# Kernel optimization log

Hardware: AMD Instinct MI355X
Metric: run time of the kernel (lower is better)

## Reference

```python
import jax, jax.numpy as jnp
import numpy as np

B, S, H, I, E = 4, 2048, 1024, 2048, 8
TOP_K = 2
INIT = 0.02


def setup_inputs() -> dict:
    key = jax.random.key(0)
    kx, kg, k1, k2, k3 = jax.random.split(key, 5)
    hidden_states = jax.random.normal(kx, (B, S, H), dtype=jnp.float32)
    gate_w = jax.random.normal(kg, (H, E), dtype=jnp.float32) * INIT
    w_gate = jax.random.normal(k1, (E, H, I), dtype=jnp.float32) * INIT  # per-expert gate_proj
    w_up = jax.random.normal(k2, (E, H, I), dtype=jnp.float32) * INIT    # per-expert up_proj
    w_down = jax.random.normal(k3, (E, I, H), dtype=jnp.float32) * INIT  # per-expert down_proj
    return {"hidden_states": hidden_states, "gate_w": gate_w,
            "w_gate": w_gate, "w_up": w_up, "w_down": w_down}


def reference(hidden_states, gate_w, w_gate, w_up, w_down):
    # Router: logits kept in float32 (original promotes to >= float32)
    router_logits = jnp.einsum('bsh,he->bse', hidden_states, gate_w).astype(jnp.float32)
    routing_weights, selected_experts = jax.lax.top_k(router_logits, k=TOP_K)
    routing_weights = jax.nn.softmax(routing_weights, axis=-1)  # [B,S,K]
    # Per-token combine weight for every expert (sum over the k slots that picked it)
    one_hot = jax.nn.one_hot(selected_experts, E, dtype=routing_weights.dtype)  # [B,S,K,E]
    combine = jnp.einsum('bske,bsk->bse', one_hot, routing_weights)  # [B,S,E]
    # Compute-all-experts dense MLP (faithful to the original per-expert loop, vectorized over E)
    gate = jax.nn.gelu(jnp.einsum('bsh,ehi->ebsi', hidden_states, w_gate), approximate=True)
    up = jnp.einsum('bsh,ehi->ebsi', hidden_states, w_up)
    expert_out = jnp.einsum('ebsi,eih->ebsh', gate * up, w_down)  # [E,B,S,H]
    final_hidden_state = jnp.einsum('bse,ebsh->bsh', combine, expert_out)
    return final_hidden_state, router_logits
```

## Files before the change

### kernel.cpp

```cpp
#include <hip/hip_runtime.h>
#include <hip/hip_bf16.h>

#define TOKENS  8192
#define HDIM    1024
#define IDIM    2048
#define NEXP    8
#define NPAIRS  16384

typedef __attribute__((ext_vector_type(8))) short bf16x8;
typedef __attribute__((ext_vector_type(4))) float f32x4;
typedef __attribute__((ext_vector_type(8))) unsigned short u16x8;

__device__ __forceinline__ unsigned short f2b(float f){
  unsigned u = __float_as_uint(f);
  u += 0x7fff + ((u >> 16) & 1);
  return (unsigned short)(u >> 16);
}

__device__ __forceinline__ void gload16(const void* g, void* l){
  __builtin_amdgcn_global_load_lds(
    (const __attribute__((address_space(1))) unsigned int*)g,
    (__attribute__((address_space(3))) unsigned int*)l, 16, 0, 0);
}

__device__ __forceinline__ float gelu_tanh(float x){
  float x3 = x*x*x;
  float t = tanhf(0.7978845608028654f*(x + 0.044715f*x3));
  return 0.5f*x*(1.0f+t);
}


__global__ void conv_hs_k(const float4* __restrict__ src, ushort4* __restrict__ dst, int n4){
  int i = blockIdx.x*blockDim.x + threadIdx.x;
  if (i >= n4) return;
  float4 v = src[i];
  ushort4 o;
  o.x = f2b(v.x); o.y = f2b(v.y); o.z = f2b(v.z); o.w = f2b(v.w);
  dst[i] = o;
}

__global__ __launch_bounds__(256)
void transpose_conv_k(const float* __restrict__ src, unsigned short* __restrict__ dst,
                      int R, int C){
  __shared__ float tile[64][65];
  size_t base = (size_t)blockIdx.z * R * C;
  const int t = threadIdx.x;
  const int x0 = blockIdx.x*64, y0 = blockIdx.y*64;
  const int rl = t >> 4, c4 = (t & 15) * 4;
  #pragma unroll
  for (int i=0;i<4;++i){
    int r = i*16 + rl;
    float4 v = *(const float4*)&src[base + (size_t)(y0 + r)*C + x0 + c4];
    tile[r][c4+0]=v.x; tile[r][c4+1]=v.y; tile[r][c4+2]=v.z; tile[r][c4+3]=v.w;
  }
  __syncthreads();
  const int c = t >> 2, r0 = (t & 3)*16;
  size_t ob = base + (size_t)(x0 + c)*R + y0;
  #pragma unroll
  for (int v=0; v<2; ++v){
    int r = r0 + v*8;
    u16x8 o;
    #pragma unroll
    for (int j=0;j<8;++j) o[j] = f2b(tile[r+j][c]);
    *(u16x8*)&dst[ob + r] = o;
  }
}


__global__ void router_k(const float* __restrict__ hs, const float* __restrict__ gw,
                         float* __restrict__ lo, int4* __restrict__ tokinfo){
  int wid  = (blockIdx.x*blockDim.x + threadIdx.x) >> 6;
  int lane = threadIdx.x & 63;
  const float* h = hs + (size_t)wid*HDIM;
  float a0=0,a1=0,a2=0,a3=0,a4=0,a5=0,a6=0,a7=0;
  for (int i = lane; i < HDIM; i += 64){
    float x = h[i];
    const float4 g0 = *(const float4*)(gw + (size_t)i*NEXP);
    const float4 g1 = *(const float4*)(gw + (size_t)i*NEXP + 4);
    a0 += x*g0.x; a1 += x*g0.y; a2 += x*g0.z; a3 += x*g0.w;
    a4 += x*g1.x; a5 += x*g1.y; a6 += x*g1.z; a7 += x*g1.w;
  }
  #pragma unroll
  for (int off = 32; off; off >>= 1){
    a0 += __shfl_xor(a0, off); a1 += __shfl_xor(a1, off);
    a2 += __shfl_xor(a2, off); a3 += __shfl_xor(a3, off);
    a4 += __shfl_xor(a4, off); a5 += __shfl_xor(a5, off);
    a6 += __shfl_xor(a6, off); a7 += __shfl_xor(a7, off);
  }
  if (lane == 0){
    float v[8] = {a0,a1,a2,a3,a4,a5,a6,a7};
    float* lp = lo + (size_t)wid*NEXP;
    #pragma unroll
    for (int e=0;e<8;++e) lp[e] = v[e];
    int e0 = 0; float b0 = v[0];
    #pragma unroll
    for (int e=1;e<8;++e){ if (v[e] > b0){ b0 = v[e]; e0 = e; } }
    int e1 = 0; float b1 = -1e30f;
    #pragma unroll
    for (int e=0;e<8;++e){ if (e != e0 && v[e] > b1){ b1 = v[e]; e1 = e; } }
    float ex = expf(b1 - b0);
    float w0 = 1.0f/(1.0f+ex);
    float w1 = ex/(1.0f+ex);
    tokinfo[wid] = make_int4(e0, e1, __float_as_int(w0), __float_as_int(w1));
  }
}

__global__ __launch_bounds__(256)
void hist_k(const int4* __restrict__ tokinfo, int* __restrict__ ctl){
  __shared__ int h[8];
  if (threadIdx.x < 8) h[threadIdx.x] = 0;
  __syncthreads();
  int4 ti = tokinfo[blockIdx.x*256 + threadIdx.x];
  atomicAdd(&h[ti.x], 1); atomicAdd(&h[ti.y], 1);
  __syncthreads();
  if (threadIdx.x < 8) atomicAdd(&ctl[threadIdx.x], h[threadIdx.x]);
}

__global__ void scan_k(int* ctl){
  if (threadIdx.x == 0){
    int s = 0;
    #pragma unroll
    for (int e=0;e<NEXP;++e){ ctl[16+e] = s; s += ctl[e]; }
  }
}

__global__ __launch_bounds__(256)
void assign_k(const int4* __restrict__ tokinfo, int* ctl,
              int* __restrict__ ptok, float* __restrict__ pw,
              int2* __restrict__ ppos){
  __shared__ int wcnt0[4][8], wcnt1[4][8];
  __shared__ int woff0[4][8], woff1[4][8];
  __shared__ int btot0[8], blkbase[8];
  const int tid = threadIdx.x, lane = tid & 63, wv = tid >> 6;
  const int tok = blockIdx.x*256 + tid;
  int4 ti = tokinfo[tok];
  const unsigned long long below = (1ull << lane) - 1ull;
  int r0 = 0, r1 = 0;
  #pragma unroll
  for (int e=0;e<8;++e){
    unsigned long long b0 = __ballot(ti.x == e);
    unsigned long long b1 = __ballot(ti.y == e);
    if (ti.x == e) r0 = __popcll(b0 & below);
    if (ti.y == e) r1 = __popcll(b1 & below);
    if (lane == 0){ wcnt0[wv][e] = __popcll(b0); wcnt1[wv][e] = __popcll(b1); }
  }
  __syncthreads();
  if (tid < 8){
    const int e = tid;
    int s0 = 0, s1 = 0;
    #pragma unroll
    for (int w=0;w<4;++w){ woff0[w][e] = s0; s0 += wcnt0[w][e]; }
    btot0[e] = s0;
    #pragma unroll
    for (int w=0;w<4;++w){ woff1[w][e] = s1; s1 += wcnt1[w][e]; }
    blkbase[e] = atomicAdd(&ctl[8+e], s0 + s1);
  }
  __syncthreads();
  const int e0 = ti.x, e1 = ti.y;
  int p0 = ctl[16+e0] + blkbase[e0] + woff0[wv][e0] + r0;
  int p1 = ctl[16+e1] + blkbase[e1] + btot0[e1] + woff1[wv][e1] + r1;
  ptok[p0] = tok; pw[p0] = __int_as_float(ti.z);
  ptok[p1] = tok; pw[p1] = __int_as_float(ti.w);
  ppos[tok] = make_int2(p0, p1);
}


__global__ __launch_bounds__(512, 2)
void moe_gateup_k(const unsigned short* __restrict__ X,
                  const unsigned short* __restrict__ WgT,
                  const unsigned short* __restrict__ WuT,
                  const int* __restrict__ ptok,
                  const int* __restrict__ ctl,
                  unsigned short* __restrict__ P){
  __shared__ unsigned short lds[2*32768];
  const int e  = blockIdx.z;
  const int wg = blockIdx.x + 32*blockIdx.y;
  const int id = (wg & 7)*64 + (wg >> 3);
  const int mt = id & 31;
  const int nt = id >> 5;
  const int cnt = ctl[e];
  if (mt*256 >= cnt) return;
  const int off = ctl[16+e];
  const int t = threadIdx.x;
  const int lane = t & 63, w = t >> 6;
  const int wr = w >> 1, wc = w & 1;

  const int r_in = t >> 3;
  const int cb   = (((t & 7) ^ (r_in & 7)) * 8);

  int tokRow[4];
  #pragma unroll
  for (int c=0;c<4;++c){
    int gm = mt*256 + c*64 + r_in;
    tokRow[c] = ptok[off + (gm < cnt ? gm : 0)];
  }
  const size_t ebase = (size_t)e * IDIM * HDIM;
  int gnRow[2];
  #pragma unroll
  for (int c=0;c<2;++c) gnRow[c] = nt*128 + c*64 + r_in;

  f32x4 accG[4][4] = {};
  f32x4 accU[4][4] = {};

  const int lq = lane >> 4, lr = lane & 15, skey = lane & 7;

  auto stage = [&](int bb, int kt){
    const int k0 = kt*64;
    #pragma unroll
    for (int c=0;c<4;++c)
      gload16(&X[(size_t)tokRow[c]*HDIM + k0 + cb], &lds[bb + c*4096 + t*8]);
    #pragma unroll
    for (int c=0;c<2;++c){
      gload16(&WgT[ebase + (size_t)gnRow[c]*HDIM + k0 + cb], &lds[bb + 16384 + c*4096 + t*8]);
      gload16(&WuT[ebase + (size_t)gnRow[c]*HDIM + k0 + cb], &lds[bb + 24576 + c*4096 + t*8]);
    }
  };

  stage(0, 0);
  __syncthreads();
  int cur = 0;
  for (int kt = 0; kt < HDIM/64; ++kt){
    if (kt < HDIM/64 - 1) stage((cur^1)*32768, kt+1);
    const int bb = cur*32768;
    #pragma unroll
    for (int kk=0;kk<2;++kk){
      const int g = ((kk*4 + lq) ^ skey) * 8;
      bf16x8 a[4], bg[4], bu[4];
      #pragma unroll
      for (int mi=0;mi<4;++mi)
        a[mi] = *(const bf16x8*)&lds[bb + (wr*64 + mi*16 + lr)*64 + g];
      #pragma unroll
      for (int ni=0;ni<4;++ni){
        bg[ni] = *(const bf16x8*)&lds[bb + 16384 + (wc*64 + ni*16 + lr)*64 + g];
        bu[ni] = *(const bf16x8*)&lds[bb + 24576 + (wc*64 + ni*16 + lr)*64 + g];
      }
      #pragma unroll
      for (int mi=0;mi<4;++mi){
        #pragma unroll
        for (int ni=0;ni<4;++ni){
          accG[mi][ni] = __builtin_amdgcn_mfma_f32_16x16x32_bf16(a[mi], bg[ni], accG[mi][ni], 0,0,0);
          accU[mi][ni] = __builtin_amdgcn_mfma_f32_16x16x32_bf16(a[mi], bu[ni], accU[mi][ni], 0,0,0);
        }
      }
    }
    __syncthreads();
    cur ^= 1;
  }

  const int rsub = (lane>>4)*4;
  const int csub = lane & 15;
  #pragma unroll
  for (int mi=0;mi<4;++mi){
    #pragma unroll
    for (int j=0;j<4;++j){
      int gm = mt*256 + wr*64 + mi*16 + rsub + j;
      if (gm >= cnt) continue;
      size_t prow = (size_t)(off+gm)*IDIM + nt*128 + wc*64 + csub;
      #pragma unroll
      for (int ni=0;ni<4;++ni){
        float g = accG[mi][ni][j];
        float u = accU[mi][ni][j];
        P[prow + ni*16] = f2b(gelu_tanh(g)*u);
      }
    }
  }
}


__global__ __launch_bounds__(512, 2)
void moe_down_k(const unsigned short* __restrict__ P,
                const unsigned short* __restrict__ WdT,
                const int* __restrict__ ctl,
                float* __restrict__ part){
  __shared__ unsigned short lds[2*24576];
  const int e  = blockIdx.z;
  const int wg = blockIdx.x + 32*blockIdx.y;
  const int id = (wg & 7)*32 + (wg >> 3);
  const int mt = id & 31;
  const int nt = id >> 5;
  const int cnt = ctl[e];
  if (mt*256 >= cnt) return;
  const int off = ctl[16+e];
  const int t = threadIdx.x;
  const int lane = t & 63, w = t >> 6;
  const int wr = w >> 1, wc = w & 1;

  const int r_in = t >> 3;
  const int cb   = (((t & 7) ^ (r_in & 7)) * 8);

  int aRow[4];
  #pragma unroll
  for (int c=0;c<4;++c){
    int gm = mt*256 + c*64 + r_in;
    aRow[c] = off + (gm < cnt ? gm : cnt-1);
  }
  const size_t ebase = (size_t)e * HDIM * IDIM;
  int gnRow[2];
  #pragma unroll
  for (int c=0;c<2;++c) gnRow[c] = nt*128 + c*64 + r_in;

  f32x4 acc[4][4] = {};

  const int lq = lane >> 4, lr = lane & 15, skey = lane & 7;

  auto stage = [&](int bb, int kt){
    const int k0 = kt*64;
    #pragma unroll
    for (int c=0;c<4;++c)
      gload16(&P[(size_t)aRow[c]*IDIM + k0 + cb], &lds[bb + c*4096 + t*8]);
    #pragma unroll
    for (int c=0;c<2;++c)
      gload16(&WdT[ebase + (size_t)gnRow[c]*IDIM + k0 + cb], &lds[bb + 16384 + c*4096 + t*8]);
  };

  stage(0, 0);
  __syncthreads();
  int cur = 0;
  for (int kt = 0; kt < IDIM/64; ++kt){
    if (kt < IDIM/64 - 1) stage((cur^1)*24576, kt+1);
    const int bb = cur*24576;
    #pragma unroll
    for (int kk=0;kk<2;++kk){
      const int g = ((kk*4 + lq) ^ skey) * 8;
      bf16x8 a[4], b[4];
      #pragma unroll
      for (int mi=0;mi<4;++mi)
        a[mi] = *(const bf16x8*)&lds[bb + (wr*64 + mi*16 + lr)*64 + g];
      #pragma unroll
      for (int ni=0;ni<4;++ni)
        b[ni] = *(const bf16x8*)&lds[bb + 16384 + (wc*64 + ni*16 + lr)*64 + g];
      #pragma unroll
      for (int mi=0;mi<4;++mi){
        #pragma unroll
        for (int ni=0;ni<4;++ni)
          acc[mi][ni] = __builtin_amdgcn_mfma_f32_16x16x32_bf16(a[mi], b[ni], acc[mi][ni], 0,0,0);
      }
    }
    __syncthreads();
    cur ^= 1;
  }

  const int rsub = (lane>>4)*4;
  const int csub = lane & 15;
  #pragma unroll
  for (int mi=0;mi<4;++mi){
    #pragma unroll
    for (int j=0;j<4;++j){
      int gm = mt*256 + wr*64 + mi*16 + rsub + j;
      if (gm >= cnt) continue;
      size_t orow = (size_t)(off+gm)*HDIM + nt*128 + wc*64 + csub;
      #pragma unroll
      for (int ni=0;ni<4;++ni)
        part[orow + ni*16] = acc[mi][ni][j];
    }
  }
}


__global__ void combine_k(const float* __restrict__ part,
                          const int2* __restrict__ ppos,
                          const float* __restrict__ pw,
                          float* __restrict__ out){
  const int tok = blockIdx.x;
  const int c4  = threadIdx.x;
  int2 p = ppos[tok];
  float w0 = pw[p.x], w1 = pw[p.y];
  float4 a = ((const float4*)(part + (size_t)p.x*HDIM))[c4];
  float4 b = ((const float4*)(part + (size_t)p.y*HDIM))[c4];
  float4 o;
  o.x = w0*a.x + w1*b.x;
  o.y = w0*a.y + w1*b.y;
  o.z = w0*a.z + w1*b.z;
  o.w = w0*a.w + w1*b.w;
  ((float4*)(out + (size_t)tok*HDIM))[c4] = o;
}


extern "C" void kernel_launch(void* const* d_in, const int* in_sizes, int n_in,
                              void* d_out, int out_size, void* d_ws, size_t ws_size,
                              hipStream_t stream){
  const float* hs     = (const float*)d_in[0];
  const float* gw     = (const float*)d_in[1];
  const float* w_gate = (const float*)d_in[2];
  const float* w_up   = (const float*)d_in[3];
  const float* w_down = (const float*)d_in[4];
  float* out_final  = (float*)d_out;
  float* out_logits = out_final + (size_t)TOKENS*HDIM;

  char* wsp = (char*)d_ws;
  int*  ctl      = (int*)wsp;
  int4* tokinfo  = (int4*)(wsp + 256);
  int*  ptok     = (int*)(wsp + 256 + TOKENS*16);
  float* pw      = (float*)(wsp + 256 + TOKENS*16 + NPAIRS*4);
  size_t o = 256 + (size_t)TOKENS*16 + (size_t)NPAIRS*8;
  o = (o + 255) & ~(size_t)255;
  int2* ppos = (int2*)(wsp + o);                    o += (size_t)TOKENS*8;
  unsigned short* hsb = (unsigned short*)(wsp + o); o += (size_t)TOKENS*HDIM*2;
  unsigned short* wgT = (unsigned short*)(wsp + o); o += (size_t)NEXP*IDIM*HDIM*2;
  unsigned short* wuT = (unsigned short*)(wsp + o); o += (size_t)NEXP*IDIM*HDIM*2;
  unsigned short* wdT = (unsigned short*)(wsp + o); o += (size_t)NEXP*HDIM*IDIM*2;
  unsigned short* P   = (unsigned short*)(wsp + o); o += (size_t)NPAIRS*IDIM*2;
  float* part = (float*)wgT;

  hipMemsetAsync(ctl, 0, 256, stream);

  conv_hs_k<<<(TOKENS*HDIM/4 + 255)/256, 256, 0, stream>>>((const float4*)hs, (ushort4*)hsb, TOKENS*HDIM/4);
  transpose_conv_k<<<dim3(IDIM/64, HDIM/64, NEXP), 256, 0, stream>>>(w_gate, wgT, HDIM, IDIM);
  transpose_conv_k<<<dim3(IDIM/64, HDIM/64, NEXP), 256, 0, stream>>>(w_up,   wuT, HDIM, IDIM);
  transpose_conv_k<<<dim3(HDIM/64, IDIM/64, NEXP), 256, 0, stream>>>(w_down, wdT, IDIM, HDIM);

  router_k<<<TOKENS/4, 256, 0, stream>>>(hs, gw, out_logits, tokinfo);
  hist_k  <<<TOKENS/256, 256, 0, stream>>>(tokinfo, ctl);
  scan_k  <<<1, 64, 0, stream>>>(ctl);
  assign_k<<<TOKENS/256, 256, 0, stream>>>(tokinfo, ctl, ptok, pw, ppos);

  moe_gateup_k<<<dim3(32, 16, NEXP), 512, 0, stream>>>(hsb, wgT, wuT, ptok, ctl, P);
  moe_down_k  <<<dim3(32, 8, NEXP), 512, 0, stream>>>(P, wdT, ctl, part);
  combine_k   <<<TOKENS, 256, 0, stream>>>(part, ppos, pw, out_final);
}
```

Measured before the change: 571.7 us.

## Shrink MoE GEMM tiles to 128x128, fuse hs conversion into router, faster GELU

The gate/up and down expert GEMMs move from 512-thread 256x128 tiles to 256-thread 128x128 tiles. The gate/up kernel also uses a K-step of 32 with a smaller LDS footprint, and the launch grids double in x. The bf16 conversion of hidden states is folded into the router kernel, which removes one launch and one extra read of the activations. The tanh GELU is rewritten in its sigmoid form using __expf, which is cheaper but may differ slightly numerically. Smaller tiles cut padding waste on uneven expert counts and raise occupancy, at the cost of more weight reloads per output.

```diff
diff --git a/kernel.cpp b/kernel.cpp
--- a/kernel.cpp
+++ b/kernel.cpp
@@ -23,20 +23,9 @@
     (__attribute__((address_space(3))) unsigned int*)l, 16, 0, 0);
 }
 
-__device__ __forceinline__ float gelu_tanh(float x){
-  float x3 = x*x*x;
-  float t = tanhf(0.7978845608028654f*(x + 0.044715f*x3));
-  return 0.5f*x*(1.0f+t);
-}
-
-
-__global__ void conv_hs_k(const float4* __restrict__ src, ushort4* __restrict__ dst, int n4){
-  int i = blockIdx.x*blockDim.x + threadIdx.x;
-  if (i >= n4) return;
-  float4 v = src[i];
-  ushort4 o;
-  o.x = f2b(v.x); o.y = f2b(v.y); o.z = f2b(v.z); o.w = f2b(v.w);
-  dst[i] = o;
+__device__ __forceinline__ float gelu_fast(float x){
+  float z2 = 1.5957691216057308f*(x + 0.044715f*x*x*x);
+  return x / (1.0f + __expf(-z2));
 }
 
 __global__ __launch_bounds__(256)
@@ -67,18 +56,29 @@
 }
 
 
-__global__ void router_k(const float* __restrict__ hs, const float* __restrict__ gw,
-                         float* __restrict__ lo, int4* __restrict__ tokinfo){
+__global__ __launch_bounds__(256)
+void router_conv_k(const float* __restrict__ hs, const float* __restrict__ gw,
+                   float* __restrict__ lo, int4* __restrict__ tokinfo,
+                   unsigned short* __restrict__ hsb){
   int wid  = (blockIdx.x*blockDim.x + threadIdx.x) >> 6;
   int lane = threadIdx.x & 63;
   const float* h = hs + (size_t)wid*HDIM;
+  unsigned short* hb = hsb + (size_t)wid*HDIM;
   float a0=0,a1=0,a2=0,a3=0,a4=0,a5=0,a6=0,a7=0;
-  for (int i = lane; i < HDIM; i += 64){
-    float x = h[i];
-    const float4 g0 = *(const float4*)(gw + (size_t)i*NEXP);
-    const float4 g1 = *(const float4*)(gw + (size_t)i*NEXP + 4);
-    a0 += x*g0.x; a1 += x*g0.y; a2 += x*g0.z; a3 += x*g0.w;
-    a4 += x*g1.x; a5 += x*g1.y; a6 += x*g1.z; a7 += x*g1.w;
+  #pragma unroll
+  for (int r=0;r<4;++r){
+    const int i0 = r*256 + lane*4;
+    float4 v = *(const float4*)&h[i0];
+    ushort4 o; o.x=f2b(v.x); o.y=f2b(v.y); o.z=f2b(v.z); o.w=f2b(v.w);
+    *(ushort4*)&hb[i0] = o;
+    float vv[4] = {v.x, v.y, v.z, v.w};
+    #pragma unroll
+    for (int j=0;j<4;++j){
+      const float4 g0 = *(const float4*)(gw + (size_t)(i0+j)*NEXP);
+      const float4 g1 = *(const float4*)(gw + (size_t)(i0+j)*NEXP + 4);
+      a0 += vv[j]*g0.x; a1 += vv[j]*g0.y; a2 += vv[j]*g0.z; a3 += vv[j]*g0.w;
+      a4 += vv[j]*g1.x; a5 += vv[j]*g1.y; a6 += vv[j]*g1.z; a7 += vv[j]*g1.w;
+    }
   }
   #pragma unroll
   for (int off = 32; off; off >>= 1){
@@ -165,33 +165,33 @@
 }
 
 
-__global__ __launch_bounds__(512, 2)
+__global__ __launch_bounds__(256, 2)
 void moe_gateup_k(const unsigned short* __restrict__ X,
                   const unsigned short* __restrict__ WgT,
                   const unsigned short* __restrict__ WuT,
                   const int* __restrict__ ptok,
                   const int* __restrict__ ctl,
                   unsigned short* __restrict__ P){
-  __shared__ unsigned short lds[2*32768];
+  __shared__ unsigned short lds[2*12288];
   const int e  = blockIdx.z;
-  const int wg = blockIdx.x + 32*blockIdx.y;
-  const int id = (wg & 7)*64 + (wg >> 3);
-  const int mt = id & 31;
-  const int nt = id >> 5;
+  const int wg = blockIdx.x + 64*blockIdx.y;
+  const int id = (wg & 7)*128 + (wg >> 3);
+  const int mt = id & 63;
+  const int nt = id >> 6;
   const int cnt = ctl[e];
-  if (mt*256 >= cnt) return;
+  if (mt*128 >= cnt) return;
   const int off = ctl[16+e];
   const int t = threadIdx.x;
   const int lane = t & 63, w = t >> 6;
   const int wr = w >> 1, wc = w & 1;
 
-  const int r_in = t >> 3;
-  const int cb   = (((t & 7) ^ (r_in & 7)) * 8);
-
-  int tokRow[4];
-  #pragma unroll
-  for (int c=0;c<4;++c){
-    int gm = mt*256 + c*64 + r_in;
+  const int r_in = t >> 2;
+  const int cb   = (((t & 3) ^ (r_in & 3)) * 8);
+
+  int tokRow[2];
+  #pragma unroll
+  for (int c=0;c<2;++c){
+    int gm = mt*128 + c*64 + r_in;
     tokRow[c] = ptok[off + (gm < cnt ? gm : 0)];
   }
   const size_t ebase = (size_t)e * IDIM * HDIM;
@@ -202,45 +202,42 @@
   f32x4 accG[4][4] = {};
   f32x4 accU[4][4] = {};
 
-  const int lq = lane >> 4, lr = lane & 15, skey = lane & 7;
+  const int lq = lane >> 4, lr = lane & 15;
 
   auto stage = [&](int bb, int kt){
-    const int k0 = kt*64;
-    #pragma unroll
-    for (int c=0;c<4;++c)
-      gload16(&X[(size_t)tokRow[c]*HDIM + k0 + cb], &lds[bb + c*4096 + t*8]);
+    const int k0 = kt*32;
+    #pragma unroll
+    for (int c=0;c<2;++c)
+      gload16(&X[(size_t)tokRow[c]*HDIM + k0 + cb], &lds[bb + c*2048 + t*8]);
     #pragma unroll
     for (int c=0;c<2;++c){
-      gload16(&WgT[ebase + (size_t)gnRow[c]*HDIM + k0 + cb], &lds[bb + 16384 + c*4096 + t*8]);
-      gload16(&WuT[ebase + (size_t)gnRow[c]*HDIM + k0 + cb], &lds[bb + 24576 + c*4096 + t*8]);
+      gload16(&WgT[ebase + (size_t)gnRow[c]*HDIM + k0 + cb], &lds[bb + 4096 + c*2048 + t*8]);
+      gload16(&WuT[ebase + (size_t)gnRow[c]*HDIM + k0 + cb], &lds[bb + 8192 + c*2048 + t*8]);
     }
   };
 
   stage(0, 0);
   __syncthreads();
   int cur = 0;
-  for (int kt = 0; kt < HDIM/64; ++kt){
-    if (kt < HDIM/64 - 1) stage((cur^1)*32768, kt+1);
-    const int bb = cur*32768;
-    #pragma unroll
-    for (int kk=0;kk<2;++kk){
-      const int g = ((kk*4 + lq) ^ skey) * 8;
-      bf16x8 a[4], bg[4], bu[4];
-      #pragma unroll
-      for (int mi=0;mi<4;++mi)
-        a[mi] = *(const bf16x8*)&lds[bb + (wr*64 + mi*16 + lr)*64 + g];
+  for (int kt = 0; kt < HDIM/32; ++kt){
+    if (kt < HDIM/32 - 1) stage((cur^1)*12288, kt+1);
+    const int bb = cur*12288;
+    const int g = ((lq ^ (lr & 3)) * 8);
+    bf16x8 a[4], bg[4], bu[4];
+    #pragma unroll
+    for (int mi=0;mi<4;++mi)
+      a[mi] = *(const bf16x8*)&lds[bb + (wr*64 + mi*16 + lr)*32 + g];
+    #pragma unroll
+    for (int ni=0;ni<4;++ni){
+      bg[ni] = *(const bf16x8*)&lds[bb + 4096 + (wc*64 + ni*16 + lr)*32 + g];
+      bu[ni] = *(const bf16x8*)&lds[bb + 8192 + (wc*64 + ni*16 + lr)*32 + g];
+    }
+    #pragma unroll
+    for (int mi=0;mi<4;++mi){
       #pragma unroll
       for (int ni=0;ni<4;++ni){
-        bg[ni] = *(const bf16x8*)&lds[bb + 16384 + (wc*64 + ni*16 + lr)*64 + g];
-        bu[ni] = *(const bf16x8*)&lds[bb + 24576 + (wc*64 + ni*16 + lr)*64 + g];
-      }
-      #pragma unroll
-      for (int mi=0;mi<4;++mi){
-        #pragma unroll
-        for (int ni=0;ni<4;++ni){
-          accG[mi][ni] = __builtin_amdgcn_mfma_f32_16x16x32_bf16(a[mi], bg[ni], accG[mi][ni], 0,0,0);
-          accU[mi][ni] = __builtin_amdgcn_mfma_f32_16x16x32_bf16(a[mi], bu[ni], accU[mi][ni], 0,0,0);
-        }
+        accG[mi][ni] = __builtin_amdgcn_mfma_f32_16x16x32_bf16(a[mi], bg[ni], accG[mi][ni], 0,0,0);
+        accU[mi][ni] = __builtin_amdgcn_mfma_f32_16x16x32_bf16(a[mi], bu[ni], accU[mi][ni], 0,0,0);
       }
     }
     __syncthreads();
@@ -253,33 +250,33 @@
   for (int mi=0;mi<4;++mi){
     #pragma unroll
     for (int j=0;j<4;++j){
-      int gm = mt*256 + wr*64 + mi*16 + rsub + j;
+      int gm = mt*128 + wr*64 + mi*16 + rsub + j;
       if (gm >= cnt) continue;
       size_t prow = (size_t)(off+gm)*IDIM + nt*128 + wc*64 + csub;
       #pragma unroll
       for (int ni=0;ni<4;++ni){
-        float g = accG[mi][ni][j];
-        float u = accU[mi][ni][j];
-        P[prow + ni*16] = f2b(gelu_tanh(g)*u);
+        float g2 = accG[mi][ni][j];
+        float u  = accU[mi][ni][j];
+        P[prow + ni*16] = f2b(gelu_fast(g2)*u);
       }
     }
   }
 }
 
 
-__global__ __launch_bounds__(512, 2)
+__global__ __launch_bounds__(256, 2)
 void moe_down_k(const unsigned short* __restrict__ P,
                 const unsigned short* __restrict__ WdT,
                 const int* __restrict__ ctl,
                 float* __restrict__ part){
-  __shared__ unsigned short lds[2*24576];
+  __shared__ unsigned short lds[2*16384];
   const int e  = blockIdx.z;
-  const int wg = blockIdx.x + 32*blockIdx.y;
-  const int id = (wg & 7)*32 + (wg >> 3);
-  const int mt = id & 31;
-  const int nt = id >> 5;
+  const int wg = blockIdx.x + 64*blockIdx.y;
+  const int id = (wg & 7)*64 + (wg >> 3);
+  const int mt = id & 63;
+  const int nt = id >> 6;
   const int cnt = ctl[e];
-  if (mt*256 >= cnt) return;
+  if (mt*128 >= cnt) return;
   const int off = ctl[16+e];
   const int t = threadIdx.x;
   const int lane = t & 63, w = t >> 6;
@@ -291,44 +288,44 @@
   int aRow[4];
   #pragma unroll
   for (int c=0;c<4;++c){
-    int gm = mt*256 + c*64 + r_in;
+    int gm = mt*128 + c*32 + r_in;
     aRow[c] = off + (gm < cnt ? gm : cnt-1);
   }
   const size_t ebase = (size_t)e * HDIM * IDIM;
-  int gnRow[2];
-  #pragma unroll
-  for (int c=0;c<2;++c) gnRow[c] = nt*128 + c*64 + r_in;
+  int gnRow[4];
+  #pragma unroll
+  for (int c=0;c<4;++c) gnRow[c] = nt*128 + c*32 + r_in;
 
   f32x4 acc[4][4] = {};
 
-  const int lq = lane >> 4, lr = lane & 15, skey = lane & 7;
+  const int lq = lane >> 4, lr = lane & 15;
 
   auto stage = [&](int bb, int kt){
     const int k0 = kt*64;
     #pragma unroll
     for (int c=0;c<4;++c)
-      gload16(&P[(size_t)aRow[c]*IDIM + k0 + cb], &lds[bb + c*4096 + t*8]);
-    #pragma unroll
-    for (int c=0;c<2;++c)
-      gload16(&WdT[ebase + (size_t)gnRow[c]*IDIM + k0 + cb], &lds[bb + 16384 + c*4096 + t*8]);
+      gload16(&P[(size_t)aRow[c]*IDIM + k0 + cb], &lds[bb + c*2048 + t*8]);
+    #pragma unroll
+    for (int c=0;c<4;++c)
+      gload16(&WdT[ebase + (size_t)gnRow[c]*IDIM + k0 + cb], &lds[bb + 8192 + c*2048 + t*8]);
   };
 
   stage(0, 0);
   __syncthreads();
   int cur = 0;
   for (int kt = 0; kt < IDIM/64; ++kt){
-    if (kt < IDIM/64 - 1) stage((cur^1)*24576, kt+1);
-    const int bb = cur*24576;
+    if (kt < IDIM/64 - 1) stage((cur^1)*16384, kt+1);
+    const int bb = cur*16384;
     #pragma unroll
     for (int kk=0;kk<2;++kk){
-      const int g = ((kk*4 + lq) ^ skey) * 8;
+      const int g = ((kk*4 + lq) ^ (lr & 7)) * 8;
       bf16x8 a[4], b[4];
       #pragma unroll
       for (int mi=0;mi<4;++mi)
         a[mi] = *(const bf16x8*)&lds[bb + (wr*64 + mi*16 + lr)*64 + g];
       #pragma unroll
       for (int ni=0;ni<4;++ni)
-        b[ni] = *(const bf16x8*)&lds[bb + 16384 + (wc*64 + ni*16 + lr)*64 + g];
+        b[ni] = *(const bf16x8*)&lds[bb + 8192 + (wc*64 + ni*16 + lr)*64 + g];
       #pragma unroll
       for (int mi=0;mi<4;++mi){
         #pragma unroll
@@ -346,7 +343,7 @@
   for (int mi=0;mi<4;++mi){
     #pragma unroll
     for (int j=0;j<4;++j){
-      int gm = mt*256 + wr*64 + mi*16 + rsub + j;
+      int gm = mt*128 + wr*64 + mi*16 + rsub + j;
       if (gm >= cnt) continue;
       size_t orow = (size_t)(off+gm)*HDIM + nt*128 + wc*64 + csub;
       #pragma unroll
@@ -404,17 +401,16 @@
 
   hipMemsetAsync(ctl, 0, 256, stream);
 
-  conv_hs_k<<<(TOKENS*HDIM/4 + 255)/256, 256, 0, stream>>>((const float4*)hs, (ushort4*)hsb, TOKENS*HDIM/4);
   transpose_conv_k<<<dim3(IDIM/64, HDIM/64, NEXP), 256, 0, stream>>>(w_gate, wgT, HDIM, IDIM);
   transpose_conv_k<<<dim3(IDIM/64, HDIM/64, NEXP), 256, 0, stream>>>(w_up,   wuT, HDIM, IDIM);
   transpose_conv_k<<<dim3(HDIM/64, IDIM/64, NEXP), 256, 0, stream>>>(w_down, wdT, IDIM, HDIM);
 
-  router_k<<<TOKENS/4, 256, 0, stream>>>(hs, gw, out_logits, tokinfo);
+  router_conv_k<<<TOKENS/4, 256, 0, stream>>>(hs, gw, out_logits, tokinfo, hsb);
   hist_k  <<<TOKENS/256, 256, 0, stream>>>(tokinfo, ctl);
   scan_k  <<<1, 64, 0, stream>>>(ctl);
   assign_k<<<TOKENS/256, 256, 0, stream>>>(tokinfo, ctl, ptok, pw, ppos);
 
-  moe_gateup_k<<<dim3(32, 16, NEXP), 512, 0, stream>>>(hsb, wgT, wuT, ptok, ctl, P);
-  moe_down_k  <<<dim3(32, 8, NEXP), 512, 0, stream>>>(P, wdT, ctl, part);
+  moe_gateup_k<<<dim3(64, 16, NEXP), 256, 0, stream>>>(hsb, wgT, wuT, ptok, ctl, P);
+  moe_down_k  <<<dim3(64, 8, NEXP), 256, 0, stream>>>(P, wdT, ctl, part);
   combine_k   <<<TOKENS, 256, 0, stream>>>(part, ppos, pw, out_final);
 }
```

Result: no change. 561.5 us (-1.8%).
